# Kernel tuning notes

Hardware: AMD Instinct MI355X
Metric: run time of the kernel (lower is better)

Reference implementation:

```python
import jax, jax.numpy as jnp
import numpy as np

HID = 128
N_LAYERS = 4


def setup_inputs() -> dict:
    key = jax.random.key(0)
    ks = jax.random.split(key, 16)
    B, T, N, F = 64, 168, 64, 17
    x = jax.random.normal(ks[0], (B, T, N, F), dtype=jnp.float32)
    adj = jax.random.randint(ks[1], (N, N), 0, 2, dtype=jnp.int32)
    s = 0.05
    W1 = jax.random.normal(ks[2], (F, HID), dtype=jnp.float32) * s
    a1 = jax.random.normal(ks[3], (2 * HID,), dtype=jnp.float32) * s
    W2 = jax.random.normal(ks[4], (HID, HID), dtype=jnp.float32) * s
    a2 = jax.random.normal(ks[5], (2 * HID,), dtype=jnp.float32) * s
    # PyTorch LSTM weights, 4 layers, gate order i,f,g,o; layer0 input=HID
    Wih = jax.random.normal(ks[6], (N_LAYERS, 4 * HID, HID), dtype=jnp.float32) * s
    Whh = jax.random.normal(ks[7], (N_LAYERS, 4 * HID, HID), dtype=jnp.float32) * s
    bih = jax.random.normal(ks[8], (N_LAYERS, 4 * HID), dtype=jnp.float32) * s
    bhh = jax.random.normal(ks[9], (N_LAYERS, 4 * HID), dtype=jnp.float32) * s
    Wlin = jax.random.normal(ks[10], (1, N_LAYERS * HID), dtype=jnp.float32) * s
    blin = jax.random.normal(ks[11], (1,), dtype=jnp.float32) * s
    return {"x": x, "adj": adj, "W1": W1, "a1": a1, "W2": W2, "a2": a2,
            "Wih": Wih, "Whh": Whh, "bih": bih, "bhh": bhh,
            "Wlin": Wlin, "blin": blin, "site_idx": 10}


def _gat(x, W, a, adj_mask):
    # x: [B,T,N,F] -> h: [B,T,N,O]; dense adjacency-masked attention
    h = jnp.einsum('btnf,fo->btno', x, W)
    O = W.shape[1]
    src = h @ a[:O]          # [B,T,N]  a^T[Wh_i || .]
    dst = h @ a[O:]          # [B,T,N]  a^T[. || Wh_j]
    e = jax.nn.leaky_relu(src[..., :, None] + dst[..., None, :], 0.2)  # [B,T,N,N]
    e = jnp.where(adj_mask, e, jnp.float32(-1e9))
    attn = jax.nn.softmax(e, axis=-1)
    return jnp.einsum('btij,btjo->btio', attn, h)


def _lstm_layer(x_seq, Wih_l, Whh_l, b_l):
    # x_seq: [B,T,H]; PyTorch gate order i,f,g,o
    B = x_seq.shape[0]
    h0 = jnp.zeros((B, HID), x_seq.dtype)

    def step(carry, x_t):
        h, c = carry
        g = x_t @ Wih_l.T + h @ Whh_l.T + b_l
        i, f, gg, o = jnp.split(g, 4, axis=-1)
        c = jax.nn.sigmoid(f) * c + jax.nn.sigmoid(i) * jnp.tanh(gg)
        h = jax.nn.sigmoid(o) * jnp.tanh(c)
        return (h, c), h

    (hT, cT), ys = jax.lax.scan(step, (h0, h0), jnp.swapaxes(x_seq, 0, 1))
    return jnp.swapaxes(ys, 0, 1), hT


def reference(x, adj, W1, a1, W2, a2, Wih, Whh, bih, bhh, Wlin, blin, site_idx):
    N = adj.shape[0]
    adj_mask = (adj > 0) | jnp.eye(N, dtype=bool)  # self-loops avoid empty rows
    h = _gat(x, W1, a1, adj_mask)
    h = _gat(h, W2, a2, adj_mask)
    seq = h[:, :, site_idx, :]                     # [B,T,HID]
    h_finals = []
    for l in range(N_LAYERS):
        seq, hT = _lstm_layer(seq, Wih[l], Whh[l], bih[l] + bhh[l])
        h_finals.append(hT)
    hcat = jnp.concatenate(h_finals, axis=-1)      # [B, 4*HID] == permute+reshape
    out = hcat @ Wlin.T + blin                     # [B,1]
    return out.squeeze(-1)
```

## Files before the change

### kernel.cpp

```cpp
#include <hip/hip_runtime.h>
#include <hip/hip_bf16.h>

#define BB 64
#define TT 168
#define NN 64
#define FF 17
#define HID 128
#define GATES 512
#define NLAYERS 4
#define NROWS (BB*TT)

#define CH 8
#define NCHUNK (TT/CH)

#define WS_W1SRC 0
#define WS_W1DST 32
#define WS_W2SRC 64
#define WS_W2DST 192
#define WS_BSUM  320
#define WS_WD    2560
#define WS_WSV   2592
#define WS_W12   2624
#define WS_WXG0T 4800
#define WS_FLAGS 16000
#define WS_XG    1395712
#define WS_HSEQ0 6900736
#define HSEQ_SZ  1376256

__device__ __forceinline__ void lds_barrier() {
    __asm__ volatile("" ::: "memory");
    __builtin_amdgcn_s_waitcnt(0xc07f);
    __builtin_amdgcn_s_barrier();
    __asm__ volatile("" ::: "memory");
}

__device__ __forceinline__ float fsig(float x) {
    return __builtin_amdgcn_rcpf(1.f + __expf(-x));
}
__device__ __forceinline__ float ftanh(float x) {
    float e = __expf(2.f * x);
    return 1.f - 2.f * __builtin_amdgcn_rcpf(e + 1.f);
}
__device__ __forceinline__ float bcast_lane(float v, int lane) {
    return __int_as_float(__builtin_amdgcn_readlane(__float_as_int(v), lane));
}

__global__ void prep1(const float* __restrict__ W1, const float* __restrict__ a1,
                      const float* __restrict__ W2, const float* __restrict__ a2,
                      const float* __restrict__ bih, const float* __restrict__ bhh,
                      float* __restrict__ ws) {
    int tid = threadIdx.x;
    if (tid < 34) {
        int f = tid % FF, half = tid / FF;
        float acc = 0.f;
        for (int o = 0; o < HID; o++) acc += W1[f*HID + o] * a1[half*HID + o];
        ws[(half ? WS_W1DST : WS_W1SRC) + f] = acc;
    }
    {
        int k = tid & 127, half = tid >> 7;
        float acc = 0.f;
        for (int o = 0; o < HID; o++) acc += W2[k*HID + o] * a2[half*HID + o];
        ws[(half ? WS_W2DST : WS_W2SRC) + k] = acc;
    }
    for (int idx = tid; idx < NLAYERS*GATES; idx += 256) ws[WS_BSUM + idx] = bih[idx] + bhh[idx];
    __hip_atomic_store((int*)(ws + WS_FLAGS) + tid, 0,
                       __ATOMIC_RELAXED, __HIP_MEMORY_SCOPE_AGENT);
}

__global__ void prep2(const float* __restrict__ W1, const float* __restrict__ W2,
                      float* __restrict__ ws) {
    int f = blockIdx.x, o = threadIdx.x;
    float acc = 0.f;
    for (int k = 0; k < HID; k++) acc += W1[f*HID + k] * W2[k*HID + o];
    ws[WS_W12 + f*HID + o] = acc;
}

__global__ void prep3(const float* __restrict__ W1, const float* __restrict__ Wih0,
                      float* __restrict__ ws) {
    int idx = blockIdx.x * 256 + threadIdx.x;
    if (idx < 17) {
        int f = idx;
        float acc = 0.f;
        for (int k = 0; k < HID; k++) acc += W1[f*HID + k] * ws[WS_W2DST + k];
        ws[WS_WD + f] = acc;
    } else if (idx < 34) {
        int f = idx - 17;
        float acc = 0.f;
        for (int k = 0; k < HID; k++) acc += W1[f*HID + k] * ws[WS_W2SRC + k];
        ws[WS_WSV + f] = acc;
    } else if (idx < 34 + GATES*FF) {
        int e = idx - 34;
        int j = e % GATES, f = e / GATES;
        float acc = 0.f;
        for (int o = 0; o < HID; o++) acc += ws[WS_W12 + f*HID + o] * Wih0[j*HID + o];
        ws[WS_WXG0T + j*20 + f] = acc;
    }
}

struct __align__(16) GatSmem {
    float attn[64*68];
    float xsT[FF*64];
    float xbarT[FF*68];
    float src1[64], dst1[64], rinv[64], att2[64];
    float xbar2[20];
    float part_x[FF*8];
    unsigned long long adjbits[64];
};

__global__ __launch_bounds__(256) void gat_fused(const float* __restrict__ x, const int* __restrict__ adj,
                                                 const float* __restrict__ ws,
                                                 float* __restrict__ Xg, const int* __restrict__ site_ptr) {
    __shared__ GatSmem sm;
    const int tid = threadIdx.x;
    const int tt = blockIdx.x, bb = blockIdx.y;
    const int site = site_ptr[0];
    const int r = bb*TT + tt;
    const float* xblk = x + (size_t)r * (NN*FF);

    for (int idx = tid; idx < NN*FF; idx += 256) {
        int n = idx / FF, f = idx % FF;
        sm.xsT[f*64 + n] = xblk[idx];
    }
    {
        int w = tid >> 6, lane = tid & 63;
        for (int rr = w*16; rr < w*16 + 16; rr++) {
            int val = adj[rr*64 + lane];
            unsigned long long m = __ballot(val > 0);
            if (lane == 0) sm.adjbits[rr] = m | (1ull << rr);
        }
    }
    lds_barrier();

    if (tid < 128) {
        int n = tid & 63, half = tid >> 6;
        const float* wv = ws + (half ? WS_W1DST : WS_W1SRC);
        float acc = 0.f;
        #pragma unroll
        for (int f = 0; f < FF; f++) acc += sm.xsT[f*64 + n] * wv[f];
        if (half) sm.dst1[n] = acc; else sm.src1[n] = acc;
    }
    lds_barrier();

    {
        int q = tid & 3, i = tid >> 2;
        unsigned long long ab = sm.adjbits[i];
        float si = sm.src1[i];
        float v[16];
        float vmax = -1e30f;
        #pragma unroll
        for (int u = 0; u < 16; u++) {
            int jj = q*16 + u;
            float e = si + sm.dst1[jj];
            float lv = fmaxf(e, 0.2f*e);
            lv = ((ab >> jj) & 1ull) ? lv : -1e9f;
            v[u] = lv;
            vmax = fmaxf(vmax, lv);
        }
        vmax = fmaxf(vmax, __shfl_xor(vmax, 1, 4));
        vmax = fmaxf(vmax, __shfl_xor(vmax, 2, 4));
        float s = 0.f;
        float* arow = &sm.attn[i*68];
        #pragma unroll
        for (int w = 0; w < 4; w++) {
            float4 pv;
            pv.x = __expf(v[w*4+0] - vmax);
            pv.y = __expf(v[w*4+1] - vmax);
            pv.z = __expf(v[w*4+2] - vmax);
            pv.w = __expf(v[w*4+3] - vmax);
            s += (pv.x + pv.y) + (pv.z + pv.w);
            *(float4*)(arow + q*16 + w*4) = pv;
        }
        s += __shfl_xor(s, 1, 4);
        s += __shfl_xor(s, 2, 4);
        if (q == 0) sm.rinv[i] = 1.f / s;
    }
    lds_barrier();

    {
        int i = tid & 63, q = tid >> 6;
        const float* arow = &sm.attn[i*68];
        float acc[5] = {0.f,0.f,0.f,0.f,0.f};
        const int nf = (q == 0) ? 5 : 4;
        for (int j4 = 0; j4 < 16; j4++) {
            float4 a4 = *(const float4*)(arow + j4*4);
            #pragma unroll
            for (int u = 0; u < 5; u++) {
                if (u < nf) {
                    int f = q + 4*u;
                    float4 x4 = *(const float4*)(&sm.xsT[f*64 + j4*4]);
                    acc[u] += a4.x*x4.x + a4.y*x4.y + a4.z*x4.z + a4.w*x4.w;
                }
            }
        }
        float ri = sm.rinv[i];
        #pragma unroll
        for (int u = 0; u < 5; u++) {
            if (u < nf) sm.xbarT[(q + 4*u)*68 + i] = acc[u] * ri;
        }
    }
    lds_barrier();

    if (tid < 64) {
        int jj = tid;
        float d = 0.f, sp = 0.f;
        #pragma unroll
        for (int f = 0; f < FF; f++) {
            float xv = sm.xbarT[f*68 + jj];
            float xs = sm.xbarT[f*68 + site];
            d  += xv * ws[WS_WD + f];
            sp += xs * ws[WS_WSV + f];
        }
        unsigned long long ab = sm.adjbits[site];
        float e = sp + d;
        float lv = fmaxf(e, 0.2f*e);
        lv = ((ab >> jj) & 1ull) ? lv : -1e9f;
        float m = lv;
        #pragma unroll
        for (int dd = 1; dd < 64; dd <<= 1) m = fmaxf(m, __shfl_xor(m, dd));
        float p = __expf(lv - m);
        float s = p;
        #pragma unroll
        for (int dd = 1; dd < 64; dd <<= 1) s += __shfl_xor(s, dd);
        sm.att2[jj] = p / s;
    }
    lds_barrier();

    if (tid < FF*8) {
        int f = tid >> 3, c = tid & 7;
        float p = 0.f;
        #pragma unroll
        for (int u = 0; u < 8; u++) {
            int i = c*8 + u;
            p += sm.att2[i] * sm.xbarT[f*68 + i];
        }
        sm.part_x[f*8 + c] = p;
    }
    lds_barrier();

    if (tid < FF) {
        float s = 0.f;
        #pragma unroll
        for (int c = 0; c < 8; c++) s += sm.part_x[tid*8 + c];
        sm.xbar2[tid] = s;
    }
    lds_barrier();

    {
        float xb[FF];
        #pragma unroll
        for (int f = 0; f < FF; f++) xb[f] = sm.xbar2[f];
        #pragma unroll
        for (int half = 0; half < 2; half++) {
            int j = tid + half*256;
            const float4* wp = (const float4*)(ws + WS_WXG0T + j*20);
            float4 w0 = wp[0], w1 = wp[1], w2 = wp[2], w3 = wp[3];
            float wlast = ws[WS_WXG0T + j*20 + 16];
            float acc = ws[WS_BSUM + j];
            acc += w0.x*xb[0] + w0.y*xb[1] + w0.z*xb[2] + w0.w*xb[3];
            acc += w1.x*xb[4] + w1.y*xb[5] + w1.z*xb[6] + w1.w*xb[7];
            acc += w2.x*xb[8] + w2.y*xb[9] + w2.z*xb[10] + w2.w*xb[11];
            acc += w3.x*xb[12] + w3.y*xb[13] + w3.z*xb[14] + w3.w*xb[15];
            acc += wlast*xb[16];
            Xg[(size_t)r*GATES + j] = acc;
        }
    }
}

__global__ __launch_bounds__(512, 1) void lstm_pipe(const float* __restrict__ Xg0,
                                                    const float* __restrict__ Wih,
                                                    const float* __restrict__ Whh,
                                                    float* __restrict__ ws) {
    const int b = blockIdx.x;
    const int l = blockIdx.y;
    const int tid = threadIdx.x;
    const int lane = tid & 63;
    const int kc = tid >> 7;
    const int jj = tid & 127;
    const int o = kc*32 + (lane & 31);
    const bool blane = (lane < 32);
    const bool storer = ((tid >> 6) & 1) == 0;

    __shared__ __align__(16) float part[2][4][128][4];
    __shared__ __align__(16) float xg[2][CH*GATES];
    __shared__ __align__(16) float xs[CH*HID];

    int* flags = (int*)(ws + WS_FLAGS);

    float w[4][32];
    {
        const float* Whh_l = Whh + (size_t)l*GATES*HID;
        #pragma unroll
        for (int u = 0; u < 4; u++) {
            const float4* wr = (const float4*)(Whh_l + (size_t)(u*128 + jj)*HID + kc*32);
            #pragma unroll
            for (int k4 = 0; k4 < 8; k4++) {
                float4 v = wr[k4];
                w[u][k4*4+0] = v.x; w[u][k4*4+1] = v.y; w[u][k4*4+2] = v.z; w[u][k4*4+3] = v.w;
            }
        }
    }

    const float* xg_g  = Xg0 + (size_t)b*TT*GATES;
    float*       hout  = ws + WS_HSEQ0 + (size_t)l*HSEQ_SZ + (size_t)b*TT*HID;
    const float* hprev = (l > 0) ? (ws + WS_HSEQ0 + (size_t)(l-1)*HSEQ_SZ + (size_t)b*TT*HID)
                                 : ws;
    const float* Wih_l = Wih + (size_t)l*GATES*HID;
    const float  bsum_j = ws[WS_BSUM + l*GATES + tid];

    float h_own = 0.f, c_own = 0.f;
    float4 pf0 = {0,0,0,0}, pf1 = {0,0,0,0};
    int buf = 0;

    if (l == 0) {
        const float4* g4 = (const float4*)xg_g;
        float4 v0 = g4[tid], v1 = g4[512 + tid];
        float4* d = (float4*)xg[0];
        d[tid] = v0; d[512 + tid] = v1;
        lds_barrier();
    }

    for (int c = 0; c < NCHUNK; c++) {
        if (l == 0) {
            if (c + 1 < NCHUNK) {
                const float4* g4 = (const float4*)(xg_g + (size_t)(c+1)*CH*GATES);
                pf0 = g4[tid]; pf1 = g4[512 + tid];
            }
        } else {
            if (tid == 0) {
                int* flg = &flags[(l-1)*BB + b];
                const int need = (c + 1)*CH;
                while (__hip_atomic_load(flg, __ATOMIC_RELAXED, __HIP_MEMORY_SCOPE_AGENT) < need)
                    __builtin_amdgcn_s_sleep(8);
            }
            lds_barrier();
            #pragma unroll
            for (int q = 0; q < 2; q++) {
                int idx = q*512 + tid;
                xs[idx] = __hip_atomic_load(&hprev[(size_t)c*CH*HID + idx],
                                            __ATOMIC_RELAXED, __HIP_MEMORY_SCOPE_AGENT);
            }
            lds_barrier();
            float acc[CH];
            #pragma unroll
            for (int t = 0; t < CH; t++) acc[t] = bsum_j;
            const float4* wr = (const float4*)(Wih_l + (size_t)tid*HID);
            #pragma unroll
            for (int kq = 0; kq < 4; kq++) {
                float4 wv[8];
                #pragma unroll
                for (int q = 0; q < 8; q++) wv[q] = wr[kq*8 + q];
                #pragma unroll
                for (int t = 0; t < CH; t++) {
                    const float4* xp = (const float4*)(xs + t*HID + kq*32);
                    float a = 0.f;
                    #pragma unroll
                    for (int q = 0; q < 8; q++) {
                        float4 xv = xp[q];
                        a += wv[q].x*xv.x + wv[q].y*xv.y + wv[q].z*xv.z + wv[q].w*xv.w;
                    }
                    acc[t] += a;
                }
            }
            #pragma unroll
            for (int t = 0; t < CH; t++) xg[0][t*GATES + tid] = acc[t];
            lds_barrier();
        }

        const float* xgbuf = xg[(l == 0) ? buf : 0];

        for (int tc = 0; tc < CH; tc++) {
            const int t = c*CH + tc;
            float xgc[4];
            if (blane) {
                #pragma unroll
                for (int u = 0; u < 4; u++) xgc[u] = xgbuf[tc*GATES + u*HID + o];
            }
            float a0 = 0.f, a1 = 0.f, a2 = 0.f, a3 = 0.f;
            #pragma unroll
            for (int k = 0; k < 32; k++) {
                float hv = bcast_lane(h_own, k);
                a0 += w[0][k]*hv; a1 += w[1][k]*hv; a2 += w[2][k]*hv; a3 += w[3][k]*hv;
            }
            float4 st = {a0, a1, a2, a3};
            *(float4*)(&part[t & 1][kc][jj][0]) = st;

            lds_barrier();

            if (blane) {
                float4 s4 = {xgc[0], xgc[1], xgc[2], xgc[3]};
                #pragma unroll
                for (int kcc = 0; kcc < 4; kcc++) {
                    float4 p = *(const float4*)(&part[t & 1][kcc][o][0]);
                    s4.x += p.x; s4.y += p.y; s4.z += p.z; s4.w += p.w;
                }
                float si = fsig(s4.x), sf = fsig(s4.y), so = fsig(s4.w);
                float tg = ftanh(s4.z);
                c_own = sf*c_own + si*tg;
                h_own = so*ftanh(c_own);
                if (storer)
                    __hip_atomic_store(&hout[t*HID + o], h_own,
                                       __ATOMIC_RELAXED, __HIP_MEMORY_SCOPE_AGENT);
            }
        }

        if (l == 0) {
            __asm__ volatile("s_waitcnt vmcnt(0)" ::: "memory");
            if (c + 1 < NCHUNK) {
                float4* d = (float4*)xg[buf ^ 1];
                d[tid] = pf0; d[512 + tid] = pf1;
                buf ^= 1;
            }
            lds_barrier();
            if (tid == 0)
                __hip_atomic_store(&flags[b], (c+1)*CH,
                                   __ATOMIC_RELAXED, __HIP_MEMORY_SCOPE_AGENT);
        } else if (l < NLAYERS - 1) {
            __asm__ volatile("s_waitcnt vmcnt(0)" ::: "memory");
            lds_barrier();
            if (tid == 0)
                __hip_atomic_store(&flags[l*BB + b], (c+1)*CH,
                                   __ATOMIC_RELAXED, __HIP_MEMORY_SCOPE_AGENT);
        }
    }
}

__global__ void final_lin(const float* __restrict__ ws, const float* __restrict__ Wlin,
                          const float* __restrict__ blin, float* __restrict__ out) {
    const int b = blockIdx.x, l = threadIdx.x;
    float acc = 0.f;
    #pragma unroll
    for (int u = 0; u < 8; u++) {
        int idx = u*64 + l;
        int layer = idx >> 7, k = idx & 127;
        const float* hs = ws + WS_HSEQ0 + (size_t)layer*HSEQ_SZ;
        acc += hs[((size_t)b*TT + (TT-1))*HID + k] * Wlin[idx];
    }
    #pragma unroll
    for (int d = 1; d < 64; d <<= 1) acc += __shfl_xor(acc, d);
    if (l == 0) out[b] = acc + blin[0];
}

extern "C" void kernel_launch(void* const* d_in, const int* in_sizes, int n_in,
                              void* d_out, int out_size, void* d_ws, size_t ws_size,
                              hipStream_t stream) {
    const float* x    = (const float*)d_in[0];
    const int*   adj  = (const int*)d_in[1];
    const float* W1   = (const float*)d_in[2];
    const float* a1   = (const float*)d_in[3];
    const float* W2   = (const float*)d_in[4];
    const float* a2   = (const float*)d_in[5];
    const float* Wih  = (const float*)d_in[6];
    const float* Whh  = (const float*)d_in[7];
    const float* bih  = (const float*)d_in[8];
    const float* bhh  = (const float*)d_in[9];
    const float* Wlin = (const float*)d_in[10];
    const float* blin = (const float*)d_in[11];
    const int*   site = (const int*)d_in[12];
    float* ws  = (float*)d_ws;
    float* out = (float*)d_out;

    prep1<<<1, 256, 0, stream>>>(W1, a1, W2, a2, bih, bhh, ws);
    prep2<<<FF, 128, 0, stream>>>(W1, W2, ws);
    prep3<<<35, 256, 0, stream>>>(W1, Wih, ws);
    gat_fused<<<dim3(TT, BB), 256, 0, stream>>>(x, adj, ws, ws + WS_XG, site);
    lstm_pipe<<<dim3(BB, NLAYERS), 512, 0, stream>>>(ws + WS_XG, Wih, Whh, ws);
    final_lin<<<64, 64, 0, stream>>>(ws, Wlin, blin, out);
}
```

Measured before the change: 680.0 us.

## Overlap next-chunk input projection with recurrent steps in layered LSTM pipeline

```diff
diff --git a/kernel.cpp b/kernel.cpp
--- a/kernel.cpp
+++ b/kernel.cpp
@@ -22,6 +22,7 @@
 #define WS_WSV   2592
 #define WS_W12   2624
 #define WS_WXG0T 4800
+#define WS_ADJB  15104
 #define WS_FLAGS 16000
 #define WS_XG    1395712
 #define WS_HSEQ0 6900736
@@ -48,7 +49,7 @@
 __global__ void prep1(const float* __restrict__ W1, const float* __restrict__ a1,
                       const float* __restrict__ W2, const float* __restrict__ a2,
                       const float* __restrict__ bih, const float* __restrict__ bhh,
-                      float* __restrict__ ws) {
+                      const int* __restrict__ adj, float* __restrict__ ws) {
     int tid = threadIdx.x;
     if (tid < 34) {
         int f = tid % FF, half = tid / FF;
@@ -63,6 +64,12 @@
         ws[(half ? WS_W2DST : WS_W2SRC) + k] = acc;
     }
     for (int idx = tid; idx < NLAYERS*GATES; idx += 256) ws[WS_BSUM + idx] = bih[idx] + bhh[idx];
+    if (tid < 64) {
+        unsigned long long m = 1ull << tid;
+        const int* ar = adj + tid*64;
+        for (int j = 0; j < 64; j++) if (ar[j] > 0) m |= (1ull << j);
+        ((unsigned long long*)(ws + WS_ADJB))[tid] = m;
+    }
     __hip_atomic_store((int*)(ws + WS_FLAGS) + tid, 0,
                        __ATOMIC_RELAXED, __HIP_MEMORY_SCOPE_AGENT);
 }
@@ -121,14 +128,7 @@
         int n = idx / FF, f = idx % FF;
         sm.xsT[f*64 + n] = xblk[idx];
     }
-    {
-        int w = tid >> 6, lane = tid & 63;
-        for (int rr = w*16; rr < w*16 + 16; rr++) {
-            int val = adj[rr*64 + lane];
-            unsigned long long m = __ballot(val > 0);
-            if (lane == 0) sm.adjbits[rr] = m | (1ull << rr);
-        }
-    }
+    if (tid < 64) sm.adjbits[tid] = ((const unsigned long long*)(ws + WS_ADJB))[tid];
     lds_barrier();
 
     if (tid < 128) {
@@ -282,7 +282,7 @@
 
     __shared__ __align__(16) float part[2][4][128][4];
     __shared__ __align__(16) float xg[2][CH*GATES];
-    __shared__ __align__(16) float xs[CH*HID];
+    __shared__ __align__(16) float xs[2][CH*HID];
 
     int* flags = (int*)(ws + WS_FLAGS);
 
@@ -291,10 +291,10 @@
         const float* Whh_l = Whh + (size_t)l*GATES*HID;
         #pragma unroll
         for (int u = 0; u < 4; u++) {
-            const float4* wr = (const float4*)(Whh_l + (size_t)(u*128 + jj)*HID + kc*32);
+            const float4* wr2 = (const float4*)(Whh_l + (size_t)(u*128 + jj)*HID + kc*32);
             #pragma unroll
             for (int k4 = 0; k4 < 8; k4++) {
-                float4 v = wr[k4];
+                float4 v = wr2[k4];
                 w[u][k4*4+0] = v.x; w[u][k4*4+1] = v.y; w[u][k4*4+2] = v.z; w[u][k4*4+3] = v.w;
             }
         }
@@ -306,10 +306,14 @@
                                  : ws;
     const float* Wih_l = Wih + (size_t)l*GATES*HID;
     const float  bsum_j = ws[WS_BSUM + l*GATES + tid];
+    const float4* wr = (const float4*)(Wih_l + (size_t)tid*HID);
 
     float h_own = 0.f, c_own = 0.f;
     float4 pf0 = {0,0,0,0}, pf1 = {0,0,0,0};
     int buf = 0;
+
+    float acc[CH];
+    float4 wv0, wv1, wv2, wv3;
 
     if (l == 0) {
         const float4* g4 = (const float4*)xg_g;
@@ -317,56 +321,75 @@
         float4* d = (float4*)xg[0];
         d[tid] = v0; d[512 + tid] = v1;
         lds_barrier();
+    } else {
+        if (tid == 0) {
+            int* flg = &flags[(l-1)*BB + b];
+            while (__hip_atomic_load(flg, __ATOMIC_RELAXED, __HIP_MEMORY_SCOPE_AGENT) < CH)
+                __builtin_amdgcn_s_sleep(8);
+        }
+        lds_barrier();
+        #pragma unroll
+        for (int q = 0; q < 2; q++) {
+            int idx = q*512 + tid;
+            xs[0][idx] = __hip_atomic_load(&hprev[idx],
+                                           __ATOMIC_RELAXED, __HIP_MEMORY_SCOPE_AGENT);
+        }
+        lds_barrier();
+        float a0[CH];
+        #pragma unroll
+        for (int t = 0; t < CH; t++) a0[t] = bsum_j;
+        #pragma unroll
+        for (int kq = 0; kq < 4; kq++) {
+            float4 wvv[8];
+            #pragma unroll
+            for (int q = 0; q < 8; q++) wvv[q] = wr[kq*8 + q];
+            #pragma unroll
+            for (int t = 0; t < CH; t++) {
+                const float4* xp = (const float4*)(&xs[0][t*HID + kq*32]);
+                float a = 0.f;
+                #pragma unroll
+                for (int q = 0; q < 8; q++) {
+                    float4 xv = xp[q];
+                    a += wvv[q].x*xv.x + wvv[q].y*xv.y + wvv[q].z*xv.z + wvv[q].w*xv.w;
+                }
+                a0[t] += a;
+            }
+        }
+        #pragma unroll
+        for (int t = 0; t < CH; t++) xg[0][t*GATES + tid] = a0[t];
+        wv0 = wr[0]; wv1 = wr[1]; wv2 = wr[2]; wv3 = wr[3];
+        #pragma unroll
+        for (int t = 0; t < CH; t++) acc[t] = bsum_j;
+        lds_barrier();
     }
 
     for (int c = 0; c < NCHUNK; c++) {
+        const bool have_next = (c + 1 < NCHUNK);
+
         if (l == 0) {
-            if (c + 1 < NCHUNK) {
+            if (have_next) {
                 const float4* g4 = (const float4*)(xg_g + (size_t)(c+1)*CH*GATES);
                 pf0 = g4[tid]; pf1 = g4[512 + tid];
             }
-        } else {
+        } else if (have_next) {
             if (tid == 0) {
                 int* flg = &flags[(l-1)*BB + b];
-                const int need = (c + 1)*CH;
+                const int need = (c + 2)*CH;
                 while (__hip_atomic_load(flg, __ATOMIC_RELAXED, __HIP_MEMORY_SCOPE_AGENT) < need)
                     __builtin_amdgcn_s_sleep(8);
             }
             lds_barrier();
-            #pragma unroll
-            for (int q = 0; q < 2; q++) {
-                int idx = q*512 + tid;
-                xs[idx] = __hip_atomic_load(&hprev[(size_t)c*CH*HID + idx],
-                                            __ATOMIC_RELAXED, __HIP_MEMORY_SCOPE_AGENT);
-            }
-            lds_barrier();
-            float acc[CH];
-            #pragma unroll
-            for (int t = 0; t < CH; t++) acc[t] = bsum_j;
-            const float4* wr = (const float4*)(Wih_l + (size_t)tid*HID);
-            #pragma unroll
-            for (int kq = 0; kq < 4; kq++) {
-                float4 wv[8];
-                #pragma unroll
-                for (int q = 0; q < 8; q++) wv[q] = wr[kq*8 + q];
-                #pragma unroll
-                for (int t = 0; t < CH; t++) {
-                    const float4* xp = (const float4*)(xs + t*HID + kq*32);
-                    float a = 0.f;
-                    #pragma unroll
-                    for (int q = 0; q < 8; q++) {
-                        float4 xv = xp[q];
-                        a += wv[q].x*xv.x + wv[q].y*xv.y + wv[q].z*xv.z + wv[q].w*xv.w;
-                    }
-                    acc[t] += a;
-                }
-            }
-            #pragma unroll
-            for (int t = 0; t < CH; t++) xg[0][t*GATES + tid] = acc[t];
-            lds_barrier();
-        }
-
-        const float* xgbuf = xg[(l == 0) ? buf : 0];
+            float v0 = __hip_atomic_load(&hprev[(size_t)(c+1)*CH*HID + tid],
+                                         __ATOMIC_RELAXED, __HIP_MEMORY_SCOPE_AGENT);
+            float v1 = __hip_atomic_load(&hprev[(size_t)(c+1)*CH*HID + 512 + tid],
+                                         __ATOMIC_RELAXED, __HIP_MEMORY_SCOPE_AGENT);
+            xs[(c+1)&1][tid] = v0;
+            xs[(c+1)&1][512 + tid] = v1;
+        }
+
+        const float* xgbuf = (l == 0) ? xg[buf] : xg[c & 1];
+        const float* xsn = xs[(c+1)&1];
+        float* xgn = xg[(c+1)&1];
 
         for (int tc = 0; tc < CH; tc++) {
             const int t = c*CH + tc;
@@ -385,6 +408,28 @@
             *(float4*)(&part[t & 1][kc][jj][0]) = st;
 
             lds_barrier();
+
+            if (l > 0 && have_next) {
+                const int kb = tc*16;
+                #pragma unroll
+                for (int t2 = 0; t2 < CH; t2++) {
+                    const float4* xp = (const float4*)(&xsn[t2*HID + kb]);
+                    float4 x0 = xp[0], x1 = xp[1], x2 = xp[2], x3 = xp[3];
+                    acc[t2] += wv0.x*x0.x + wv0.y*x0.y + wv0.z*x0.z + wv0.w*x0.w
+                             + wv1.x*x1.x + wv1.y*x1.y + wv1.z*x1.z + wv1.w*x1.w
+                             + wv2.x*x2.x + wv2.y*x2.y + wv2.z*x2.z + wv2.w*x2.w
+                             + wv3.x*x3.x + wv3.y*x3.y + wv3.z*x3.z + wv3.w*x3.w;
+                }
+                const int ns = (tc + 1) & 7;
+                wv0 = wr[ns*4+0]; wv1 = wr[ns*4+1]; wv2 = wr[ns*4+2]; wv3 = wr[ns*4+3];
+                if (tc == CH-1) {
+                    #pragma unroll
+                    for (int t2 = 0; t2 < CH; t2++) {
+                        xgn[t2*GATES + tid] = acc[t2];
+                        acc[t2] = bsum_j;
+                    }
+                }
+            }
 
             if (blane) {
                 float4 s4 = {xgc[0], xgc[1], xgc[2], xgc[3]};
@@ -405,7 +450,7 @@
 
         if (l == 0) {
             __asm__ volatile("s_waitcnt vmcnt(0)" ::: "memory");
-            if (c + 1 < NCHUNK) {
+            if (have_next) {
                 float4* d = (float4*)xg[buf ^ 1];
                 d[tid] = pf0; d[512 + tid] = pf1;
                 buf ^= 1;
@@ -414,10 +459,10 @@
             if (tid == 0)
                 __hip_atomic_store(&flags[b], (c+1)*CH,
                                    __ATOMIC_RELAXED, __HIP_MEMORY_SCOPE_AGENT);
-        } else if (l < NLAYERS - 1) {
+        } else {
             __asm__ volatile("s_waitcnt vmcnt(0)" ::: "memory");
             lds_barrier();
-            if (tid == 0)
+            if (l < NLAYERS - 1 && tid == 0)
                 __hip_atomic_store(&flags[l*BB + b], (c+1)*CH,
                                    __ATOMIC_RELAXED, __HIP_MEMORY_SCOPE_AGENT);
         }
@@ -459,7 +504,7 @@
     float* ws  = (float*)d_ws;
     float* out = (float*)d_out;
 
-    prep1<<<1, 256, 0, stream>>>(W1, a1, W2, a2, bih, bhh, ws);
+    prep1<<<1, 256, 0, stream>>>(W1, a1, W2, a2, bih, bhh, adj, ws);
     prep2<<<FF, 128, 0, stream>>>(W1, W2, ws);
     prep3<<<35, 256, 0, stream>>>(W1, Wih, ws);
     gat_fused<<<dim3(TT, BB), 256, 0, stream>>>(x, adj, ws, ws + WS_XG, site);
```

Result: faster. 586.7 us (-13.7%).
